# Kernel optimization log

Hardware: AMD Instinct MI355X
Metric: run time of the kernel (lower is better)

The kernel has to match this reference:

```python
import jax, jax.numpy as jnp
import numpy as np

BETA = 0.25
N_EMBED = 8192
DIM = 256


def setup_inputs() -> dict:
    key = jax.random.key(0)
    k1, k2 = jax.random.split(key)
    z = jax.random.normal(k1, (16, DIM, 32, 32), dtype=jnp.float32)
    # nn.Embedding init: uniform(-1/n_embed, 1/n_embed)
    codebook = jax.random.uniform(
        k2, (N_EMBED, DIM), dtype=jnp.float32,
        minval=-1.0 / N_EMBED, maxval=1.0 / N_EMBED)
    return {"z": z, "codebook": codebook}


def reference(z, codebook):
    # b c h w -> b h w c
    zp = jnp.transpose(z, (0, 2, 3, 1))
    b, h, w, c = zp.shape
    zf = zp.reshape(-1, c)  # [N, dim]
    # squared L2 distances: ||z||^2 + ||e||^2 - 2 z.e
    d = (jnp.sum(zf * zf, axis=1, keepdims=True)
         + jnp.sum(codebook * codebook, axis=1)
         - 2.0 * jnp.einsum('nd,kd->nk', zf, codebook))  # [N, n_embed]
    idx = jnp.argmin(d, axis=1)  # [N]
    z_q = codebook[idx].reshape(b, h, w, c)
    loss = (BETA * jnp.mean((jax.lax.stop_gradient(z_q) - zp) ** 2)
            + jnp.mean((z_q - jax.lax.stop_gradient(zp)) ** 2))
    # straight-through estimator
    z_q = zp + jax.lax.stop_gradient(z_q - zp)
    z_q = jnp.transpose(z_q, (0, 3, 1, 2))  # b h w c -> b c h w
    return z_q, loss, idx
```

## Files before the change

### kernel.cpp

```cpp
#include <hip/hip_runtime.h>
#include <cfloat>


#define NROWS 16384
#define NCODE 8192
#define DIMC  256
#define HW    1024
#define ZQN   4194304

#define ZT_OFF   0
#define CBT_OFF  2097152
#define CAND_OFF 3145728
#define LOSS_OFF ZQN
#define IDX_OFF  (ZQN + 1)

#define NSLICE 8
#define CAND_BYTES ((size_t)NSLICE * NROWS * 4 * sizeof(unsigned))
#define PRUNE_T 4300u
#define ZSCALE 2097152.0f

typedef __attribute__((ext_vector_type(8))) short bf16x8;
typedef __attribute__((ext_vector_type(4))) float f32x4;
typedef __attribute__((ext_vector_type(4))) unsigned int uint4v;

__device__ __forceinline__ unsigned umax(unsigned a, unsigned b) { return a > b ? a : b; }
__device__ __forceinline__ unsigned umin(unsigned a, unsigned b) { return a < b ? a : b; }

__device__ __forceinline__ unsigned short f2bf(float f) {
    unsigned u = __float_as_uint(f);
    return (unsigned short)((u + 0x7fffu + ((u >> 16) & 1u)) >> 16);
}

#define GLD_LDS16(gptr, lptr) \
  __builtin_amdgcn_global_load_lds((const __attribute__((address_space(1))) unsigned int*)(const void*)(gptr), \
                                   (__attribute__((address_space(3))) unsigned int*)(lptr), 16, 0, 0)

__global__ void prep_kernel(const float* __restrict__ z, const float* __restrict__ cb,
                            float* __restrict__ out) {
    int bid = blockIdx.x;
    int tid = threadIdx.x;
    if (bid < 1024) {
        __shared__ unsigned short lds[64 * 65];
        unsigned short* zt = (unsigned short*)(out + ZT_OFF);
        int c0 = (bid & 3) * 64;
        int n0 = (bid >> 2) * 64;
        const float* zb = z + (size_t)(n0 >> 10) * (DIMC * HW) + (n0 & 1023);
        #pragma unroll
        for (int i = 0; i < 4; ++i) {
            int f = tid + i * 256;
            int cl = f >> 4, n4 = f & 15;
            float4 v = *(const float4*)(zb + (size_t)(c0 + cl) * HW + n4 * 4);
            lds[(n4 * 4 + 0) * 65 + cl] = f2bf(v.x * ZSCALE);
            lds[(n4 * 4 + 1) * 65 + cl] = f2bf(v.y * ZSCALE);
            lds[(n4 * 4 + 2) * 65 + cl] = f2bf(v.z * ZSCALE);
            lds[(n4 * 4 + 3) * 65 + cl] = f2bf(v.w * ZSCALE);
        }
        __syncthreads();
        #pragma unroll
        for (int i = 0; i < 2; ++i) {
            int f = tid + i * 256;
            int nl = f >> 3, oct = f & 7;
            const unsigned short* p = lds + nl * 65 + oct * 8;
            uint4v u;
            u.x = (unsigned)p[0] | ((unsigned)p[1] << 16);
            u.y = (unsigned)p[2] | ((unsigned)p[3] << 16);
            u.z = (unsigned)p[4] | ((unsigned)p[5] << 16);
            u.w = (unsigned)p[6] | ((unsigned)p[7] << 16);
            *(uint4v*)(zt + (size_t)(n0 + nl) * DIMC + c0 + oct * 8) = u;
        }
    } else {
        unsigned short* cbt = (unsigned short*)(out + CBT_OFF);
        size_t t = (size_t)(bid - 1024) * 256 + tid;
        float4 a = *(const float4*)(cb + t * 8);
        float4 b = *(const float4*)(cb + t * 8 + 4);
        uint4v u;
        u.x = (unsigned)f2bf(a.x) | ((unsigned)f2bf(a.y) << 16);
        u.y = (unsigned)f2bf(a.z) | ((unsigned)f2bf(a.w) << 16);
        u.z = (unsigned)f2bf(b.x) | ((unsigned)f2bf(b.y) << 16);
        u.w = (unsigned)f2bf(b.z) | ((unsigned)f2bf(b.w) << 16);
        *(uint4v*)(cbt + t * 8) = u;
        if (bid == 1024 && tid == 0) out[LOSS_OFF] = 0.0f;
    }
}

__global__ __launch_bounds__(256, 2)
void argmin_kernel(const float* __restrict__ out, unsigned* __restrict__ cand) {
    __shared__ __align__(16) unsigned short a_s[2 * 32 * 256];
    const unsigned short* zt  = (const unsigned short*)(out + ZT_OFF);
    const unsigned short* cbt = (const unsigned short*)(out + CBT_OFF);

    int tid = threadIdx.x;
    int lane = tid & 63;
    int wv = tid >> 6;
    int col = lane & 15, qk = lane >> 4;
    int n0 = blockIdx.x * 256;
    int slice = blockIdx.y;

    bf16x8 B[4][8];
    #pragma unroll
    for (int rf = 0; rf < 4; ++rf)
        #pragma unroll
        for (int t = 0; t < 8; ++t)
            B[rf][t] = *(const bf16x8*)(zt + (size_t)(n0 + wv * 64 + rf * 16 + col) * DIMC
                                           + t * 32 + qk * 8);

    int rl2 = lane >> 5;
    int jsl = lane & 31;
    const unsigned short* srcb[4];
    #pragma unroll
    for (int c = 0; c < 4; ++c) {
        int rloc = (wv * 4 + c) * 2 + rl2;
        int src16 = jsl ^ (rloc & 7) ^ ((rloc & 8) >> 1);
        srcb[c] = cbt + ((size_t)slice * 1024 + rloc) * DIMC + src16 * 8;
    }

    unsigned U1[4] = {0, 0, 0, 0}, U2[4] = {0, 0, 0, 0};

    const unsigned sb = (unsigned)((col & 7) ^ ((col & 8) >> 1));
    const unsigned short* aoff[8];
    #pragma unroll
    for (int t = 0; t < 8; ++t)
        aoff[t] = a_s + col * 256 + (((unsigned)(qk + 4 * t)) ^ sb) * 8;

    f32x4 acc[4][2];
    const f32x4 BIASV = (f32x4){131072.0f, 131072.0f, 131072.0f, 131072.0f};

    auto stage = [&](int ch, int dsto ) {
        const size_t off = (size_t)ch * 32 * DIMC;
        unsigned short* dst = a_s + dsto;
        #pragma unroll
        for (int c = 0; c < 4; ++c)
            GLD_LDS16(srcb[c] + off, dst + (wv * 4 + c) * 512);
    };

    auto epi1 = [&](unsigned tb) {
        #pragma unroll
        for (int rf = 0; rf < 4; ++rf)
            #pragma unroll
            for (int r = 0; r < 4; ++r) {
                unsigned bits = __float_as_uint(acc[rf][1][r]);
                unsigned u = (bits & 0xFFFFFF00u) | (tb - (unsigned)(4 + r));
                unsigned lo = umin(u, U1[rf]);
                U1[rf] = umax(u, U1[rf]);
                U2[rf] = umax(lo, U2[rf]);
            }
    };

    auto compute = [&](int bufb , unsigned tb) {
        #pragma unroll
        for (int rf = 0; rf < 4; ++rf) acc[rf][0] = BIASV;
        #pragma unroll
        for (int t = 0; t < 8; ++t) {
            bf16x8 af = *(const bf16x8*)((const char*)aoff[t] + bufb);
            acc[0][0] = __builtin_amdgcn_mfma_f32_16x16x32_bf16(af, B[0][t], acc[0][0], 0, 0, 0);
            acc[1][0] = __builtin_amdgcn_mfma_f32_16x16x32_bf16(af, B[1][t], acc[1][0], 0, 0, 0);
            acc[2][0] = __builtin_amdgcn_mfma_f32_16x16x32_bf16(af, B[2][t], acc[2][0], 0, 0, 0);
            acc[3][0] = __builtin_amdgcn_mfma_f32_16x16x32_bf16(af, B[3][t], acc[3][0], 0, 0, 0);
        }
        #pragma unroll
        for (int rf = 0; rf < 4; ++rf) acc[rf][1] = BIASV;
        #pragma unroll
        for (int t = 0; t < 8; ++t) {
            bf16x8 af = *(const bf16x8*)((const char*)aoff[t] + bufb + 8192);
            acc[0][1] = __builtin_amdgcn_mfma_f32_16x16x32_bf16(af, B[0][t], acc[0][1], 0, 0, 0);
            acc[1][1] = __builtin_amdgcn_mfma_f32_16x16x32_bf16(af, B[1][t], acc[1][1], 0, 0, 0);
            acc[2][1] = __builtin_amdgcn_mfma_f32_16x16x32_bf16(af, B[2][t], acc[2][1], 0, 0, 0);
            acc[3][1] = __builtin_amdgcn_mfma_f32_16x16x32_bf16(af, B[3][t], acc[3][1], 0, 0, 0);
            {
                const int q0 = 2 * t, q1 = 2 * t + 1;
                const int rfA = q0 >> 2, rA = q0 & 3;
                const int rfB = q1 >> 2, rB = q1 & 3;
                unsigned bitsA = __float_as_uint(acc[rfA][0][rA]);
                unsigned uA = (bitsA & 0xFFFFFF00u) | (tb - (unsigned)rA);
                unsigned loA = umin(uA, U1[rfA]);
                U1[rfA] = umax(uA, U1[rfA]);
                U2[rfA] = umax(loA, U2[rfA]);
                unsigned bitsB = __float_as_uint(acc[rfB][0][rB]);
                unsigned uB = (bitsB & 0xFFFFFF00u) | (tb - (unsigned)rB);
                unsigned loB = umin(uB, U1[rfB]);
                U1[rfB] = umax(uB, U1[rfB]);
                U2[rfB] = umax(loB, U2[rfB]);
            }
        }
    };

    stage(0, 0);
    __syncthreads();
    stage(1, 8192);
    compute(0, 255u);

    #pragma unroll 1
    for (int k = 0; k < 15; ++k) {
        const int c1 = 2 * k + 1;
        const unsigned tb = 255u - ((unsigned)c1 << 3);
        __syncthreads();
        stage(c1 + 1, 0);
        epi1(tb + 8u);
        compute(16384, tb);
        __syncthreads();
        stage(c1 + 2, 8192);
        epi1(tb);
        compute(0, tb - 8u);
    }
    __syncthreads();
    epi1(255u - (30u << 3));
    compute(16384, 255u - (31u << 3));
    epi1(255u - (31u << 3));

    #pragma unroll
    for (int rf = 0; rf < 4; ++rf) {
        unsigned t1 = 255u - (U1[rf] & 255u);
        unsigned c1 = (t1 >> 3) * 32 + ((t1 >> 2) & 1) * 16 + qk * 4 + (t1 & 3);
        unsigned x1 = ((((U1[rf] & 0xFFFFFF00u) - 0x47000000u) >> 3) << 10) | (1023u - c1);
        unsigned t2 = 255u - (U2[rf] & 255u);
        unsigned c2 = (t2 >> 3) * 32 + ((t2 >> 2) & 1) * 16 + qk * 4 + (t2 & 3);
        unsigned x2 = ((((U2[rf] & 0xFFFFFF00u) - 0x47000000u) >> 3) << 10) | (1023u - c2);
        unsigned p1 = __shfl_xor(x1, 16);
        unsigned p2 = __shfl_xor(x2, 16);
        unsigned s1 = umax(x1, p1), tm = umin(x1, p1);
        unsigned ym = umax(x2, p2), s4 = umin(x2, p2);
        unsigned s2 = umax(tm, ym), s3 = umin(tm, ym);
        unsigned r1 = umax(s1, __shfl_xor(s4, 32));
        unsigned r2 = umax(s2, __shfl_xor(s3, 32));
        unsigned r3 = umax(s3, __shfl_xor(s2, 32));
        unsigned r4 = umax(s4, __shfl_xor(s1, 32));
        if (qk == 0) {
            int row = wv * 64 + rf * 16 + col;
            uint4v cw; cw.x = r1; cw.y = r2; cw.z = r3; cw.w = r4;
            *(uint4v*)(cand + ((size_t)slice * NROWS + n0 + row) * 4) = cw;
        }
    }
}

__global__ __launch_bounds__(256, 2)
void fixup_kernel(const float* __restrict__ z, const float* __restrict__ cb,
                  float* __restrict__ out, const unsigned* __restrict__ cand,
                  int fuse_zq) {
    __shared__ float zs[32 * 264];
    __shared__ double dp[8][32];
    __shared__ float zsq_s[32];
    __shared__ unsigned qmx[32];
    __shared__ float dsc[32 * 33];
    __shared__ unsigned cds[32 * 33];
    __shared__ unsigned wl[1024];
    __shared__ unsigned wl_n;
    __shared__ unsigned bcode[32];
    __shared__ double lred[4];
    int tid = threadIdx.x;
    int n0 = blockIdx.x * 32;
    const float* zb = z + (size_t)(n0 >> 10) * (DIMC * HW) + (n0 & 1023);

    {
        int q = tid & 7, cq = tid >> 3;
        #pragma unroll
        for (int i = 0; i < 8; ++i) {
            int c = cq + i * 32;
            float4 v = *(const float4*)(zb + (size_t)c * HW + q * 4);
            int sc = c ^ (q << 2);
            zs[(q * 4 + 0) * 264 + sc] = v.x;
            zs[(q * 4 + 1) * 264 + sc] = v.y;
            zs[(q * 4 + 2) * 264 + sc] = v.z;
            zs[(q * 4 + 3) * 264 + sc] = v.w;
        }
    }
    if (tid < 32) qmx[tid] = 0;
    if (tid == 0) wl_n = 0;

    int j = tid >> 3, r = tid & 7;
    unsigned w[4];
    #pragma unroll
    for (int b = 0; b < 4; ++b)
        w[b] = cand[(((size_t)(j >> 2)) * NROWS + n0 + b * 8 + r) * 4 + (j & 3)];
    __syncthreads();

    {
        int row = tid & 31, cg = tid >> 5;
        const float* zrow = zs + row * 264;
        const int xr = (row >> 2) << 2;
        double s = 0.0;
        #pragma unroll
        for (int i = 0; i < 8; ++i) {
            int c = cg * 32 + i * 4;
            float4 zv = *(const float4*)(zrow + (c ^ xr));
            s += (double)zv.x * (double)zv.x + (double)zv.y * (double)zv.y
               + (double)zv.z * (double)zv.z + (double)zv.w * (double)zv.w;
        }
        dp[cg][row] = s;
    }
    #pragma unroll
    for (int b = 0; b < 4; ++b)
        atomicMax(&qmx[b * 8 + r], w[b] >> 10);
    for (int i = tid; i < 32 * 33; i += 256) { dsc[i] = FLT_MAX; cds[i] = 0xffffffffu; }
    __syncthreads();
    if (tid < 32) {
        double s = ((dp[0][tid] + dp[1][tid]) + (dp[2][tid] + dp[3][tid]))
                 + ((dp[4][tid] + dp[5][tid]) + (dp[6][tid] + dp[7][tid]));
        zsq_s[tid] = (float)s;
    }
    #pragma unroll
    for (int b = 0; b < 4; ++b) {
        int row = b * 8 + r;
        unsigned qv = w[b] >> 10;
        if (qv + PRUNE_T >= qmx[row]) {
            unsigned code = (unsigned)((j >> 2) * 1024) + 1023u - (w[b] & 1023u);
            unsigned e = ((unsigned)row << 18) | ((unsigned)j << 13) | code;
            unsigned pos = atomicAdd(&wl_n, 1u);
            wl[pos] = e;
        }
    }
    __syncthreads();

    {
        int g = tid >> 3, l8 = tid & 7;
        int L = (int)wl_n;
        for (int base = 0; base < L; base += 32) {
            int idx = base + g;
            double part = 0.0;
            int row = 0, jj = 0;
            unsigned code = 0;
            if (idx < L) {
                unsigned e = wl[idx];
                row = (int)(e >> 18); jj = (int)((e >> 13) & 31u);
                code = e & 8191u;
                const float* eb = cb + (size_t)code * DIMC;
                const float* zrow = zs + row * 264;
                const int xr = (row >> 2) << 2;
                #pragma unroll
                for (int k = 0; k < 8; ++k) {
                    int c = k * 32 + l8 * 4;
                    float4 ev = *(const float4*)(eb + c);
                    float4 zv = *(const float4*)(zrow + (c ^ xr));
                    part += (double)zv.x * (double)ev.x + (double)zv.y * (double)ev.y
                          + (double)zv.z * (double)ev.z + (double)zv.w * (double)ev.w;
                }
            }
            part += __shfl_xor(part, 1);
            part += __shfl_xor(part, 2);
            part += __shfl_xor(part, 4);
            if (idx < L && l8 == 0) {
                dsc[row * 33 + jj] = fmaf(-2.0f, (float)part, zsq_s[row]);
                cds[row * 33 + jj] = code;
            }
        }
    }
    __syncthreads();
    if (tid < 32) {
        float bd = FLT_MAX; unsigned bi = 0xffffffffu;
        for (int jj = 0; jj < 32; ++jj) {
            float dv = dsc[tid * 33 + jj];
            unsigned k = cds[tid * 33 + jj];
            if (dv < bd || (dv == bd && k < bi)) { bd = dv; bi = k; }
        }
        out[IDX_OFF + n0 + tid] = (float)bi;
        bcode[tid] = bi;
    }
    __syncthreads();

    {
        int row = tid & 31, cg = tid >> 5;
        const float* zrow = zs + row * 264;
        const int xr = (row >> 2) << 2;
        const float* e = cb + (size_t)bcode[row] * DIMC;
        double lacc = 0.0;
        #pragma unroll
        for (int i = 0; i < 8; ++i) {
            int c = cg * 32 + (((i + row) & 7) << 2);
            float4 ev = *(const float4*)(e + c);
            float4 zv = *(const float4*)(zrow + (c ^ xr));
            double d0 = (double)ev.x - (double)zv.x;
            double d1 = (double)ev.y - (double)zv.y;
            double d2 = (double)ev.z - (double)zv.z;
            double d3 = (double)ev.w - (double)zv.w;
            lacc += d0 * d0 + d1 * d1 + d2 * d2 + d3 * d3;
        }
        #pragma unroll
        for (int off = 32; off; off >>= 1) lacc += __shfl_down(lacc, off);
        if ((tid & 63) == 0) lred[tid >> 6] = lacc;
    }
    __syncthreads();
    if (tid == 0) {
        double part = (lred[0] + lred[1]) + (lred[2] + lred[3]);
        atomicAdd(out + LOSS_OFF, (float)(part * (1.25 / 4194304.0)));
    }

    if (fuse_zq) {
        {
            int rr = tid >> 3, q = tid & 7;
            const float* e = cb + (size_t)bcode[rr] * DIMC;
            #pragma unroll
            for (int i = 0; i < 8; ++i) {
                int c = i * 32 + q * 4;
                *(float4*)(zs + rr * 264 + c) = *(const float4*)(e + c);
            }
        }
        __syncthreads();
        int hwq = tid & 7, ch0 = tid >> 3;
        int bb = n0 >> 10, hw0 = n0 & 1023;
        float* zqbase = out + (size_t)bb * (DIMC * HW) + hw0 + hwq * 4;
        #pragma unroll
        for (int i = 0; i < 8; ++i) {
            int c = ch0 + i * 32;
            float4 v;
            v.x = zs[(hwq * 4 + 0) * 264 + c];
            v.y = zs[(hwq * 4 + 1) * 264 + c];
            v.z = zs[(hwq * 4 + 2) * 264 + c];
            v.w = zs[(hwq * 4 + 3) * 264 + c];
            *(float4*)(zqbase + (size_t)c * HW) = v;
        }
    }
}

__global__ __launch_bounds__(256)
void zq_kernel(const float* __restrict__ z, const float* __restrict__ cb,
               float* __restrict__ out) {
    __shared__ float lds[16 * 260];
    int tid = threadIdx.x;
    int n0 = blockIdx.x * 16;
    {
        int rr = tid >> 4, q = tid & 15;
        int code = (int)out[IDX_OFF + n0 + rr];
        const float* e = cb + (size_t)code * DIMC;
        #pragma unroll
        for (int jj = 0; jj < 4; ++jj) {
            int c = q * 4 + jj * 64;
            *(float4*)(lds + rr * 260 + c) = *(const float4*)(e + c);
        }
    }
    __syncthreads();
    int g = tid >> 2, rq = tid & 3;
    int b = n0 >> 10, hw0 = n0 & 1023;
    const size_t base = (size_t)b * (DIMC * HW) + hw0 + rq * 4;
    #pragma unroll
    for (int i = 0; i < 4; ++i) {
        int c = g + i * 64;
        float4 v;
        v.x = lds[(rq * 4 + 0) * 260 + c];
        v.y = lds[(rq * 4 + 1) * 260 + c];
        v.z = lds[(rq * 4 + 2) * 260 + c];
        v.w = lds[(rq * 4 + 3) * 260 + c];
        *(float4*)(out + base + (size_t)c * HW) = v;
    }
}

extern "C" void kernel_launch(void* const* d_in, const int* in_sizes, int n_in,
                              void* d_out, int out_size, void* d_ws, size_t ws_size,
                              hipStream_t stream) {
    const float* z  = (const float*)d_in[0];
    const float* cb = (const float*)d_in[1];
    float* out = (float*)d_out;

    const bool fuse = (d_ws != nullptr) && (ws_size >= CAND_BYTES);
    unsigned* candp = fuse ? (unsigned*)d_ws : (unsigned*)(out + CAND_OFF);

    prep_kernel<<<2048, 256, 0, stream>>>(z, cb, out);
    argmin_kernel<<<dim3(64, NSLICE), 256, 0, stream>>>(out, candp);
    fixup_kernel<<<512, 256, 0, stream>>>(z, cb, out, candp, fuse ? 1 : 0);
    if (!fuse)
        zq_kernel<<<1024, 256, 0, stream>>>(z, cb, out);
}
```

Before: 156.5 us.

## Fuse prep, argmin and fixup into one cooperative kernel with grid syncs

Merges the three kernels into a single cooperative launch of 512 blocks that runs prep, argmin and fixup in turn, separated by grid-wide syncs and sharing one LDS buffer. The aim is to remove the launch gaps and tail drain between kernels. The trade-off is that the fused kernel must fit the largest LDS and register footprint of all three phases, which can cut occupancy. Prep is also restricted to 512 resident blocks looping over its work. If the cooperative launch fails, it falls back to the separate launches.

```diff
diff --git a/kernel.cpp b/kernel.cpp
--- a/kernel.cpp
+++ b/kernel.cpp
@@ -1,4 +1,5 @@
 #include <hip/hip_runtime.h>
+#include <hip/hip_cooperative_groups.h>
 #include <cfloat>
 
 
@@ -19,6 +20,8 @@
 #define PRUNE_T 4300u
 #define ZSCALE 2097152.0f
 
+namespace cg = cooperative_groups;
+
 typedef __attribute__((ext_vector_type(8))) short bf16x8;
 typedef __attribute__((ext_vector_type(4))) float f32x4;
 typedef __attribute__((ext_vector_type(4))) unsigned int uint4v;
@@ -35,12 +38,24 @@
   __builtin_amdgcn_global_load_lds((const __attribute__((address_space(1))) unsigned int*)(const void*)(gptr), \
                                    (__attribute__((address_space(3))) unsigned int*)(lptr), 16, 0, 0)
 
-__global__ void prep_kernel(const float* __restrict__ z, const float* __restrict__ cb,
-                            float* __restrict__ out) {
-    int bid = blockIdx.x;
-    int tid = threadIdx.x;
+struct FixS {
+    float zs[32 * 264];
+    double dp[8][32];
+    double lred[4];
+    float zsq_s[32];
+    float dsc[32 * 33];
+    unsigned qmx[32];
+    unsigned cds[32 * 33];
+    unsigned wl[1024];
+    unsigned bcode[32];
+    unsigned wl_n;
+};
+
+
+__device__ __forceinline__ void prep_body(int bid, int tid,
+        const float* __restrict__ z, const float* __restrict__ cb,
+        float* __restrict__ out, unsigned short* lds ) {
     if (bid < 1024) {
-        __shared__ unsigned short lds[64 * 65];
         unsigned short* zt = (unsigned short*)(out + ZT_OFF);
         int c0 = (bid & 3) * 64;
         int n0 = (bid >> 2) * 64;
@@ -68,6 +83,7 @@
             u.w = (unsigned)p[6] | ((unsigned)p[7] << 16);
             *(uint4v*)(zt + (size_t)(n0 + nl) * DIMC + c0 + oct * 8) = u;
         }
+        __syncthreads();
     } else {
         unsigned short* cbt = (unsigned short*)(out + CBT_OFF);
         size_t t = (size_t)(bid - 1024) * 256 + tid;
@@ -83,18 +99,16 @@
     }
 }
 
-__global__ __launch_bounds__(256, 2)
-void argmin_kernel(const float* __restrict__ out, unsigned* __restrict__ cand) {
-    __shared__ __align__(16) unsigned short a_s[2 * 32 * 256];
+__device__ __forceinline__ void argmin_body(int rb, int slice, int tid,
+        const float* __restrict__ out, unsigned* __restrict__ cand,
+        unsigned short* a_s ) {
     const unsigned short* zt  = (const unsigned short*)(out + ZT_OFF);
     const unsigned short* cbt = (const unsigned short*)(out + CBT_OFF);
 
-    int tid = threadIdx.x;
     int lane = tid & 63;
     int wv = tid >> 6;
     int col = lane & 15, qk = lane >> 4;
-    int n0 = blockIdx.x * 256;
-    int slice = blockIdx.y;
+    int n0 = rb * 256;
 
     bf16x8 B[4][8];
     #pragma unroll
@@ -232,22 +246,11 @@
     }
 }
 
-__global__ __launch_bounds__(256, 2)
-void fixup_kernel(const float* __restrict__ z, const float* __restrict__ cb,
-                  float* __restrict__ out, const unsigned* __restrict__ cand,
-                  int fuse_zq) {
-    __shared__ float zs[32 * 264];
-    __shared__ double dp[8][32];
-    __shared__ float zsq_s[32];
-    __shared__ unsigned qmx[32];
-    __shared__ float dsc[32 * 33];
-    __shared__ unsigned cds[32 * 33];
-    __shared__ unsigned wl[1024];
-    __shared__ unsigned wl_n;
-    __shared__ unsigned bcode[32];
-    __shared__ double lred[4];
-    int tid = threadIdx.x;
-    int n0 = blockIdx.x * 32;
+__device__ __forceinline__ void fixup_body(int bidx, int tid,
+        const float* __restrict__ z, const float* __restrict__ cb,
+        float* __restrict__ out, const unsigned* __restrict__ cand,
+        int fuse_zq, FixS& S) {
+    int n0 = bidx * 32;
     const float* zb = z + (size_t)(n0 >> 10) * (DIMC * HW) + (n0 & 1023);
 
     {
@@ -257,14 +260,14 @@
             int c = cq + i * 32;
             float4 v = *(const float4*)(zb + (size_t)c * HW + q * 4);
             int sc = c ^ (q << 2);
-            zs[(q * 4 + 0) * 264 + sc] = v.x;
-            zs[(q * 4 + 1) * 264 + sc] = v.y;
-            zs[(q * 4 + 2) * 264 + sc] = v.z;
-            zs[(q * 4 + 3) * 264 + sc] = v.w;
-        }
-    }
-    if (tid < 32) qmx[tid] = 0;
-    if (tid == 0) wl_n = 0;
+            S.zs[(q * 4 + 0) * 264 + sc] = v.x;
+            S.zs[(q * 4 + 1) * 264 + sc] = v.y;
+            S.zs[(q * 4 + 2) * 264 + sc] = v.z;
+            S.zs[(q * 4 + 3) * 264 + sc] = v.w;
+        }
+    }
+    if (tid < 32) S.qmx[tid] = 0;
+    if (tid == 0) S.wl_n = 0;
 
     int j = tid >> 3, r = tid & 7;
     unsigned w[4];
@@ -274,56 +277,56 @@
     __syncthreads();
 
     {
-        int row = tid & 31, cg = tid >> 5;
-        const float* zrow = zs + row * 264;
+        int row = tid & 31, cg2 = tid >> 5;
+        const float* zrow = S.zs + row * 264;
         const int xr = (row >> 2) << 2;
         double s = 0.0;
         #pragma unroll
         for (int i = 0; i < 8; ++i) {
-            int c = cg * 32 + i * 4;
+            int c = cg2 * 32 + i * 4;
             float4 zv = *(const float4*)(zrow + (c ^ xr));
             s += (double)zv.x * (double)zv.x + (double)zv.y * (double)zv.y
                + (double)zv.z * (double)zv.z + (double)zv.w * (double)zv.w;
         }
-        dp[cg][row] = s;
+        S.dp[cg2][row] = s;
     }
     #pragma unroll
     for (int b = 0; b < 4; ++b)
-        atomicMax(&qmx[b * 8 + r], w[b] >> 10);
-    for (int i = tid; i < 32 * 33; i += 256) { dsc[i] = FLT_MAX; cds[i] = 0xffffffffu; }
+        atomicMax(&S.qmx[b * 8 + r], w[b] >> 10);
+    for (int i = tid; i < 32 * 33; i += 256) { S.dsc[i] = FLT_MAX; S.cds[i] = 0xffffffffu; }
     __syncthreads();
     if (tid < 32) {
-        double s = ((dp[0][tid] + dp[1][tid]) + (dp[2][tid] + dp[3][tid]))
-                 + ((dp[4][tid] + dp[5][tid]) + (dp[6][tid] + dp[7][tid]));
-        zsq_s[tid] = (float)s;
+        double s = ((S.dp[0][tid] + S.dp[1][tid]) + (S.dp[2][tid] + S.dp[3][tid]))
+                 + ((S.dp[4][tid] + S.dp[5][tid]) + (S.dp[6][tid] + S.dp[7][tid]));
+        S.zsq_s[tid] = (float)s;
     }
     #pragma unroll
     for (int b = 0; b < 4; ++b) {
         int row = b * 8 + r;
         unsigned qv = w[b] >> 10;
-        if (qv + PRUNE_T >= qmx[row]) {
+        if (qv + PRUNE_T >= S.qmx[row]) {
             unsigned code = (unsigned)((j >> 2) * 1024) + 1023u - (w[b] & 1023u);
             unsigned e = ((unsigned)row << 18) | ((unsigned)j << 13) | code;
-            unsigned pos = atomicAdd(&wl_n, 1u);
-            wl[pos] = e;
+            unsigned pos = atomicAdd(&S.wl_n, 1u);
+            S.wl[pos] = e;
         }
     }
     __syncthreads();
 
     {
         int g = tid >> 3, l8 = tid & 7;
-        int L = (int)wl_n;
+        int L = (int)S.wl_n;
         for (int base = 0; base < L; base += 32) {
             int idx = base + g;
             double part = 0.0;
             int row = 0, jj = 0;
             unsigned code = 0;
             if (idx < L) {
-                unsigned e = wl[idx];
+                unsigned e = S.wl[idx];
                 row = (int)(e >> 18); jj = (int)((e >> 13) & 31u);
                 code = e & 8191u;
                 const float* eb = cb + (size_t)code * DIMC;
-                const float* zrow = zs + row * 264;
+                const float* zrow = S.zs + row * 264;
                 const int xr = (row >> 2) << 2;
                 #pragma unroll
                 for (int k = 0; k < 8; ++k) {
@@ -338,8 +341,8 @@
             part += __shfl_xor(part, 2);
             part += __shfl_xor(part, 4);
             if (idx < L && l8 == 0) {
-                dsc[row * 33 + jj] = fmaf(-2.0f, (float)part, zsq_s[row]);
-                cds[row * 33 + jj] = code;
+                S.dsc[row * 33 + jj] = fmaf(-2.0f, (float)part, S.zsq_s[row]);
+                S.cds[row * 33 + jj] = code;
             }
         }
     }
@@ -347,24 +350,24 @@
     if (tid < 32) {
         float bd = FLT_MAX; unsigned bi = 0xffffffffu;
         for (int jj = 0; jj < 32; ++jj) {
-            float dv = dsc[tid * 33 + jj];
-            unsigned k = cds[tid * 33 + jj];
+            float dv = S.dsc[tid * 33 + jj];
+            unsigned k = S.cds[tid * 33 + jj];
             if (dv < bd || (dv == bd && k < bi)) { bd = dv; bi = k; }
         }
         out[IDX_OFF + n0 + tid] = (float)bi;
-        bcode[tid] = bi;
+        S.bcode[tid] = bi;
     }
     __syncthreads();
 
     {
-        int row = tid & 31, cg = tid >> 5;
-        const float* zrow = zs + row * 264;
+        int row = tid & 31, cg2 = tid >> 5;
+        const float* zrow = S.zs + row * 264;
         const int xr = (row >> 2) << 2;
-        const float* e = cb + (size_t)bcode[row] * DIMC;
+        const float* e = cb + (size_t)S.bcode[row] * DIMC;
         double lacc = 0.0;
         #pragma unroll
         for (int i = 0; i < 8; ++i) {
-            int c = cg * 32 + (((i + row) & 7) << 2);
+            int c = cg2 * 32 + (((i + row) & 7) << 2);
             float4 ev = *(const float4*)(e + c);
             float4 zv = *(const float4*)(zrow + (c ^ xr));
             double d0 = (double)ev.x - (double)zv.x;
@@ -375,22 +378,22 @@
         }
         #pragma unroll
         for (int off = 32; off; off >>= 1) lacc += __shfl_down(lacc, off);
-        if ((tid & 63) == 0) lred[tid >> 6] = lacc;
+        if ((tid & 63) == 0) S.lred[tid >> 6] = lacc;
     }
     __syncthreads();
     if (tid == 0) {
-        double part = (lred[0] + lred[1]) + (lred[2] + lred[3]);
+        double part = (S.lred[0] + S.lred[1]) + (S.lred[2] + S.lred[3]);
         atomicAdd(out + LOSS_OFF, (float)(part * (1.25 / 4194304.0)));
     }
 
     if (fuse_zq) {
         {
             int rr = tid >> 3, q = tid & 7;
-            const float* e = cb + (size_t)bcode[rr] * DIMC;
+            const float* e = cb + (size_t)S.bcode[rr] * DIMC;
             #pragma unroll
             for (int i = 0; i < 8; ++i) {
                 int c = i * 32 + q * 4;
-                *(float4*)(zs + rr * 264 + c) = *(const float4*)(e + c);
+                *(float4*)(S.zs + rr * 264 + c) = *(const float4*)(e + c);
             }
         }
         __syncthreads();
@@ -401,13 +404,52 @@
         for (int i = 0; i < 8; ++i) {
             int c = ch0 + i * 32;
             float4 v;
-            v.x = zs[(hwq * 4 + 0) * 264 + c];
-            v.y = zs[(hwq * 4 + 1) * 264 + c];
-            v.z = zs[(hwq * 4 + 2) * 264 + c];
-            v.w = zs[(hwq * 4 + 3) * 264 + c];
+            v.x = S.zs[(hwq * 4 + 0) * 264 + c];
+            v.y = S.zs[(hwq * 4 + 1) * 264 + c];
+            v.z = S.zs[(hwq * 4 + 2) * 264 + c];
+            v.w = S.zs[(hwq * 4 + 3) * 264 + c];
             *(float4*)(zqbase + (size_t)c * HW) = v;
         }
     }
+}
+
+__global__ __launch_bounds__(256, 2)
+void vq_fused(const float* __restrict__ z, const float* __restrict__ cb,
+              float* __restrict__ out, unsigned* __restrict__ cand, int fuse_zq) {
+    __shared__ __align__(16) unsigned char smem[sizeof(FixS)];
+    cg::grid_group grid = cg::this_grid();
+    const int bx = blockIdx.x;
+    const int tid = threadIdx.x;
+
+    #pragma unroll 1
+    for (int v = bx; v < 2048; v += 512)
+        prep_body(v, tid, z, cb, out, (unsigned short*)smem);
+    grid.sync();
+
+    argmin_body(bx & 63, bx >> 6, tid, out, cand, (unsigned short*)smem);
+    grid.sync();
+
+    fixup_body(bx, tid, z, cb, out, cand, fuse_zq, *(FixS*)smem);
+}
+
+__global__ void prep_kernel(const float* __restrict__ z, const float* __restrict__ cb,
+                            float* __restrict__ out) {
+    __shared__ unsigned short lds[64 * 65];
+    prep_body(blockIdx.x, threadIdx.x, z, cb, out, lds);
+}
+
+__global__ __launch_bounds__(256, 2)
+void argmin_kernel(const float* __restrict__ out, unsigned* __restrict__ cand) {
+    __shared__ __align__(16) unsigned short a_s[2 * 32 * 256];
+    argmin_body(blockIdx.x, blockIdx.y, threadIdx.x, out, cand, a_s);
+}
+
+__global__ __launch_bounds__(256, 2)
+void fixup_kernel(const float* __restrict__ z, const float* __restrict__ cb,
+                  float* __restrict__ out, const unsigned* __restrict__ cand,
+                  int fuse_zq) {
+    __shared__ __align__(16) unsigned char smem[sizeof(FixS)];
+    fixup_body(blockIdx.x, threadIdx.x, z, cb, out, cand, fuse_zq, *(FixS*)smem);
 }
 
 __global__ __launch_bounds__(256)
@@ -451,10 +493,16 @@
 
     const bool fuse = (d_ws != nullptr) && (ws_size >= CAND_BYTES);
     unsigned* candp = fuse ? (unsigned*)d_ws : (unsigned*)(out + CAND_OFF);
-
-    prep_kernel<<<2048, 256, 0, stream>>>(z, cb, out);
-    argmin_kernel<<<dim3(64, NSLICE), 256, 0, stream>>>(out, candp);
-    fixup_kernel<<<512, 256, 0, stream>>>(z, cb, out, candp, fuse ? 1 : 0);
+    int fz = fuse ? 1 : 0;
+
+    void* args[] = {(void*)&z, (void*)&cb, (void*)&out, (void*)&candp, (void*)&fz};
+    hipError_t e = hipLaunchCooperativeKernel((const void*)vq_fused,
+                                              dim3(512), dim3(256), args, 0, stream);
+    if (e != hipSuccess) {
+        prep_kernel<<<2048, 256, 0, stream>>>(z, cb, out);
+        argmin_kernel<<<dim3(64, NSLICE), 256, 0, stream>>>(out, candp);
+        fixup_kernel<<<512, 256, 0, stream>>>(z, cb, out, candp, fz);
+    }
     if (!fuse)
         zq_kernel<<<1024, 256, 0, stream>>>(z, cb, out);
 }
```

Result: slower. 280.4 us (+79.1%).
